# Performance work log

Hardware: AMD Instinct MI355X
Metric: run time of the kernel (lower is better)

The kernel has to match this reference:

```python
import jax, jax.numpy as jnp
import numpy as np

B, L, DIM, H, HD = 2, 2048, 1024, 16, 64


def _rope_tables(L, hd):
    inv_freq = 1.0 / (10000.0 ** (np.arange(0, hd, 2, dtype=np.float32) / hd))
    t = np.arange(L, dtype=np.float32)
    freqs = np.outer(t, inv_freq)                 # [L, hd/2]
    emb = np.concatenate([freqs, freqs], axis=-1)  # [L, hd]
    return jnp.asarray(np.cos(emb)), jnp.asarray(np.sin(emb))


def setup_inputs() -> dict:
    key = jax.random.key(0)
    k1, k2, k3 = jax.random.split(key, 3)
    x = jax.random.normal(k1, (B, L, DIM), dtype=jnp.float32)
    cos, sin = _rope_tables(L, HD)
    w_qkv = jax.random.normal(k2, (DIM, 3 * H * HD), dtype=jnp.float32) * (DIM ** -0.5)
    w_out = jax.random.normal(k3, (H * HD, DIM), dtype=jnp.float32) * ((H * HD) ** -0.5)
    return {"x": x, "cos": cos, "sin": sin, "w_qkv": w_qkv, "w_out": w_out}


def _rotate_half(u):
    u1, u2 = jnp.split(u, 2, axis=-1)
    return jnp.concatenate([-u2, u1], axis=-1)


def _apply_rope(u, cos, sin):
    # u: [B, L, H, hd]; cos/sin: [L, hd]
    c = cos[None, :, None, :]
    s = sin[None, :, None, :]
    return u * c + _rotate_half(u) * s


def reference(x, cos, sin, w_qkv, w_out):
    b, l, _ = x.shape
    qkv = jnp.einsum('bld,de->ble', x, w_qkv).reshape(b, l, 3 * H, HD)
    q, k, v = jnp.split(qkv, 3, axis=2)          # each [B, L, H, hd]
    q = _apply_rope(q, cos, sin)
    k = _apply_rope(k, cos, sin)
    scale = HD ** -0.5                            # SDPA default scale
    scores = jnp.einsum('bqhd,bkhd->bhqk', q, k) * scale
    attn = jax.nn.softmax(scores, axis=-1)
    o = jnp.einsum('bhqk,bkhd->bqhd', attn, v).reshape(b, l, H * HD)
    return jnp.einsum('ble,ed->bld', o, w_out)
```

## Files before the change

### kernel.cpp

```cpp
#include <hip/hip_runtime.h>
#include <hip/hip_bf16.h>

#define BATCH 2
#define SEQ   2048
#define DIM   1024
#define NH    16
#define HD    64
#define K_DIM 1024

typedef __attribute__((ext_vector_type(8))) short short8;
typedef __attribute__((ext_vector_type(4))) short short4v;
typedef __attribute__((ext_vector_type(4))) float f32x4;
typedef unsigned short ushort_t;

__device__ __forceinline__ unsigned short f2b(float x) {
    unsigned int u = __float_as_uint(x);
    u += 0x7FFFu + ((u >> 16) & 1u);
    return (unsigned short)(u >> 16);
}

#define ASYNC_COPY16(gp, lp) \
    __builtin_amdgcn_global_load_lds((const __attribute__((address_space(1))) void*)(gp), \
                                     (__attribute__((address_space(3))) void*)(lp), 16, 0, 0)

__global__ __launch_bounds__(256)
void prep(const float* __restrict__ x, const float* __restrict__ w_qkv,
          const float* __restrict__ w_out, ushort_t* __restrict__ xb,
          ushort_t* __restrict__ wqb, ushort_t* __restrict__ wob)
{
    const int bid = blockIdx.x;
    if (bid < 1024) {
        constexpr int n4 = (BATCH * SEQ * DIM) / 4;
        int i = bid * 256 + threadIdx.x;
        for (; i < n4; i += 1024 * 256) {
            float4 v = ((const float4*)x)[i];
            short4v o;
            o[0] = (short)f2b(v.x); o[1] = (short)f2b(v.y);
            o[2] = (short)f2b(v.z); o[3] = (short)f2b(v.w);
            ((short4v*)xb)[i] = o;
        }
    } else {
        const int lane = threadIdx.x & 63;
        const float* src; ushort_t* dst; int N, job;
        if (bid < 2560) { src = w_qkv; dst = wqb; N = 3072; job = (bid - 1024) * 4 + (threadIdx.x >> 6); }
        else            { src = w_out; dst = wob; N = 1024; job = (bid - 2560) * 4 + (threadIdx.x >> 6); }
        const int jn = (N == 3072) ? (job % 48) : (job % 16);
        const int jk = (N == 3072) ? (job / 48) : (job / 16);
        const int n  = jn * 64 + lane;
        const int k0 = jk * 8;
        short8 o;
        #pragma unroll
        for (int j = 0; j < 8; ++j) o[j] = (short)f2b(src[(size_t)(k0 + j) * N + n]);
        *(short8*)(dst + (size_t)n * K_DIM + k0) = o;
    }
}

__device__ __forceinline__ void gemm_stage(const ushort_t* __restrict__ Ag,
                                           const ushort_t* __restrict__ Bg,
                                           ushort_t* As, ushort_t* Bs,
                                           int k0, int w, int r0, int c0)
{
    ASYNC_COPY16(Ag + (size_t)r0 * K_DIM + k0 + c0 * 8,        As + w * 512);
    ASYNC_COPY16(Ag + (size_t)(64 + r0) * K_DIM + k0 + c0 * 8, As + w * 512 + 2048);
    ASYNC_COPY16(Bg + (size_t)r0 * K_DIM + k0 + c0 * 8,        Bs + w * 512);
    ASYNC_COPY16(Bg + (size_t)(64 + r0) * K_DIM + k0 + c0 * 8, Bs + w * 512 + 2048);
}

__device__ __forceinline__ void mfma_gemm_tile(
    const ushort_t* __restrict__ Ag, const ushort_t* __restrict__ Bg,
    ushort_t (&As)[2][128 * 32], ushort_t (&Bs)[2][128 * 32], f32x4 acc[4][4])
{
    const int t = threadIdx.x;
    const int w = t >> 6, lane = t & 63;
    const int qd = lane >> 4, cl = lane & 15;
    const int p0 = w * 64 + lane;
    const int r0 = p0 >> 2;
    const int c0 = (p0 & 3) ^ (r0 & 3);

    gemm_stage(Ag, Bg, As[0], Bs[0], 0, w, r0, c0);

    for (int kt = 0; kt < K_DIM / 32; ++kt) {
        const int cur = kt & 1;
        __syncthreads();
        if (kt + 1 < K_DIM / 32)
            gemm_stage(Ag, Bg, As[cur ^ 1], Bs[cur ^ 1], (kt + 1) * 32, w, r0, c0);

        short8 af[4], bfr[4];
        #pragma unroll
        for (int rt = 0; rt < 4; ++rt) {
            const int row = (w >> 1) * 64 + rt * 16 + cl;
            af[rt] = *(const short8*)(As[cur] + row * 32 + ((qd ^ (row & 3)) * 8));
        }
        #pragma unroll
        for (int ct = 0; ct < 4; ++ct) {
            const int col = (w & 1) * 64 + ct * 16 + cl;
            bfr[ct] = *(const short8*)(Bs[cur] + col * 32 + ((qd ^ (col & 3)) * 8));
        }
        #pragma unroll
        for (int rt = 0; rt < 4; ++rt)
            #pragma unroll
            for (int ct = 0; ct < 4; ++ct)
                acc[rt][ct] = __builtin_amdgcn_mfma_f32_16x16x32_bf16(
                    af[rt], bfr[ct], acc[rt][ct], 0, 0, 0);
    }
}

__global__ __launch_bounds__(256, 3)
void gemm_qkv_mfma(const ushort_t* __restrict__ xb, const ushort_t* __restrict__ wqb,
                   ushort_t* __restrict__ qb, ushort_t* __restrict__ kb,
                   ushort_t* __restrict__ vt,
                   const float* __restrict__ cosb, const float* __restrict__ sinb)
{
    __shared__ __align__(16) ushort_t As[2][128 * 32];
    __shared__ __align__(16) ushort_t Bs[2][128 * 32];
    const int m0 = blockIdx.y * 128, n0 = blockIdx.x * 128;

    f32x4 acc[4][4];
    #pragma unroll
    for (int i = 0; i < 4; ++i)
        #pragma unroll
        for (int j = 0; j < 4; ++j)
            #pragma unroll
            for (int r = 0; r < 4; ++r) acc[i][j][r] = 0.f;

    mfma_gemm_tile(xb + (size_t)m0 * K_DIM, wqb + (size_t)n0 * K_DIM, As, Bs, acc);

    const int t = threadIdx.x, w = t >> 6, lane = t & 63;
    const int qd = lane >> 4, cl = lane & 15;
    const int b = m0 >> 11;
    const int lbase = (m0 & 2047) + (w >> 1) * 64;
    const int region = blockIdx.x >> 3;
    const int h = (blockIdx.x & 7) * 2 + (w & 1);

    if (region < 2) {
        ushort_t* dst = region ? kb : qb;
        const float sc = region ? 1.0f : 0.18033688011111234f;
        #pragma unroll
        for (int rt = 0; rt < 4; ++rt) {
            #pragma unroll
            for (int r = 0; r < 4; ++r) {
                const int l = lbase + rt * 16 + qd * 4 + r;
                const float c0 = cosb[l * HD + cl],      s0 = sinb[l * HD + cl];
                const float c1 = cosb[l * HD + 16 + cl], s1 = sinb[l * HD + 16 + cl];
                const float v0 = acc[rt][0][r] * c0 - acc[rt][2][r] * s0;
                const float v1 = acc[rt][1][r] * c1 - acc[rt][3][r] * s1;
                const float v2 = acc[rt][2][r] * c0 + acc[rt][0][r] * s0;
                const float v3 = acc[rt][3][r] * c1 + acc[rt][1][r] * s1;
                short4v o4;
                o4[0] = (short)f2b(v0 * sc);
                o4[1] = (short)f2b(v1 * sc);
                o4[2] = (short)f2b(v2 * sc);
                o4[3] = (short)f2b(v3 * sc);
                *(short4v*)(dst + (((size_t)b * NH + h) * SEQ + l) * HD + cl * 4) = o4;
            }
        }
    } else {
        #pragma unroll
        for (int rt = 0; rt < 4; ++rt)
            #pragma unroll
            for (int ct = 0; ct < 4; ++ct) {
                const int d = ct * 16 + cl;
                const int l = lbase + rt * 16 + qd * 4;
                short4v o4;
                #pragma unroll
                for (int r = 0; r < 4; ++r) o4[r] = (short)f2b(acc[rt][ct][r]);
                *(short4v*)(vt + (((size_t)b * NH + h) * HD + d) * SEQ + l) = o4;
            }
    }
}

__device__ __forceinline__ void go_stage(const ushort_t* __restrict__ Ag,
                                         const ushort_t* __restrict__ Bg,
                                         ushort_t* As, ushort_t* Bs,
                                         int k0, int w, int lane)
{
    #pragma unroll
    for (int j = 0; j < 2; ++j) {
        const int r = w * 32 + j * 16 + (lane >> 2);
        const int c = (lane & 3) ^ (r & 3);
        ASYNC_COPY16(Ag + (size_t)r * K_DIM + k0 + c * 8, As + (w * 128 + j * 64) * 8);
    }
    const int rb = w * 16 + (lane >> 2);
    const int cb = (lane & 3) ^ (rb & 3);
    ASYNC_COPY16(Bg + (size_t)rb * K_DIM + k0 + cb * 8, Bs + (w * 64) * 8);
}

__global__ __launch_bounds__(256, 3)
void gemm_out_mfma(const ushort_t* __restrict__ ob, const ushort_t* __restrict__ wob,
                   float* __restrict__ out)
{
    __shared__ __align__(16) ushort_t As[2][128 * 32];
    __shared__ __align__(16) ushort_t Bs[2][64 * 32];
    const int m0 = blockIdx.y * 128, n0 = blockIdx.x * 64;
    const int t = threadIdx.x;
    const int w = t >> 6, lane = t & 63;
    const int qd = lane >> 4, cl = lane & 15;
    const int wr = w >> 1, wc = w & 1;

    f32x4 acc[4][2];
    #pragma unroll
    for (int i = 0; i < 4; ++i)
        #pragma unroll
        for (int j = 0; j < 2; ++j)
            #pragma unroll
            for (int r = 0; r < 4; ++r) acc[i][j][r] = 0.f;

    const ushort_t* Ag = ob  + (size_t)m0 * K_DIM;
    const ushort_t* Bg = wob + (size_t)n0 * K_DIM;
    go_stage(Ag, Bg, As[0], Bs[0], 0, w, lane);

    for (int kt = 0; kt < K_DIM / 32; ++kt) {
        const int cur = kt & 1;
        __syncthreads();
        if (kt + 1 < K_DIM / 32)
            go_stage(Ag, Bg, As[cur ^ 1], Bs[cur ^ 1], (kt + 1) * 32, w, lane);

        short8 af[4], bfr[2];
        #pragma unroll
        for (int rt = 0; rt < 4; ++rt) {
            const int row = wr * 64 + rt * 16 + cl;
            af[rt] = *(const short8*)(As[cur] + row * 32 + ((qd ^ (row & 3)) * 8));
        }
        #pragma unroll
        for (int ct = 0; ct < 2; ++ct) {
            const int col = wc * 32 + ct * 16 + cl;
            bfr[ct] = *(const short8*)(Bs[cur] + col * 32 + ((qd ^ (col & 3)) * 8));
        }
        #pragma unroll
        for (int rt = 0; rt < 4; ++rt)
            #pragma unroll
            for (int ct = 0; ct < 2; ++ct)
                acc[rt][ct] = __builtin_amdgcn_mfma_f32_16x16x32_bf16(
                    af[rt], bfr[ct], acc[rt][ct], 0, 0, 0);
    }

    const int mbase = m0 + wr * 64, nbase = n0 + wc * 32;
    #pragma unroll
    for (int rt = 0; rt < 4; ++rt)
        #pragma unroll
        for (int ct = 0; ct < 2; ++ct)
            #pragma unroll
            for (int r = 0; r < 4; ++r)
                out[(size_t)(mbase + rt * 16 + qd * 4 + r) * DIM + nbase + ct * 16 + cl] =
                    acc[rt][ct][r];
}

__global__ __launch_bounds__(256, 2)
void attn_mfma(const ushort_t* __restrict__ qb, const ushort_t* __restrict__ kb,
               const ushort_t* __restrict__ vt, ushort_t* __restrict__ ob)
{
    const int h = blockIdx.x;
    const int b = blockIdx.y;
    const int qt = blockIdx.z;
    const int t = threadIdx.x;
    const int w = t >> 6, lane = t & 63;
    const int qd = lane >> 4, cl = lane & 15;
    constexpr int NT = SEQ / 64;

    __shared__ __align__(16) ushort_t Ks[2][64 * 64];
    __shared__ __align__(16) ushort_t Vs[2][64 * 64];

    const size_t bh = (size_t)b * NH + h;
    const ushort_t* qbase = qb + (bh * SEQ + qt * 128 + w * 32) * HD;
    const ushort_t* kbase = kb + bh * SEQ * HD;
    const ushort_t* vbase = vt + bh * (size_t)HD * SEQ;

    const int p0 = w * 128 + lane;
    const int r0a = p0 >> 3,  c0a = (p0 & 7) ^ (r0a & 7);
    const int p1 = p0 + 64;
    const int r1a = p1 >> 3,  c1a = (p1 & 7) ^ (r1a & 7);
    const int ldsoff0 = (w * 128) * 8;
    const int ldsoff1 = (w * 128 + 64) * 8;

    const ushort_t* kg0 = kbase + (size_t)r0a * HD + c0a * 8;
    const ushort_t* kg1 = kbase + (size_t)r1a * HD + c1a * 8;
    const ushort_t* vg0 = vbase + (size_t)r0a * SEQ + c0a * 8;
    const ushort_t* vg1 = vbase + (size_t)r1a * SEQ + c1a * 8;

    const int lo0 = (cl * 8 + (qd ^ (cl & 7))) * 8;
    const int lo1 = (cl * 8 + ((4 + qd) ^ (cl & 7))) * 8;
    const ushort_t* kE0 = Ks[0] + lo0; const ushort_t* kE1 = Ks[0] + lo1;
    const ushort_t* vE0 = Vs[0] + lo0; const ushort_t* vE1 = Vs[0] + lo1;
    const ushort_t* kO0 = Ks[1] + lo0; const ushort_t* kO1 = Ks[1] + lo1;
    const ushort_t* vO0 = Vs[1] + lo0; const ushort_t* vO1 = Vs[1] + lo1;

    short8 qf[2][2];
    #pragma unroll
    for (int nt = 0; nt < 2; ++nt)
        #pragma unroll
        for (int kh = 0; kh < 2; ++kh)
            qf[nt][kh] = *(const short8*)(qbase + (nt * 16 + cl) * HD + kh * 32 + qd * 8);

    const f32x4 fz = {0.f, 0.f, 0.f, 0.f};
    short8 onesA;
    #pragma unroll
    for (int e = 0; e < 8; ++e) onesA[e] = (short)0x3F80;

    f32x4 oaccT[4][2];
    f32x4 lacc[2];
    #pragma unroll
    for (int dt = 0; dt < 4; ++dt)
        #pragma unroll
        for (int nt = 0; nt < 2; ++nt)
            #pragma unroll
            for (int r = 0; r < 4; ++r) oaccT[dt][nt][r] = 0.f;
    #pragma unroll
    for (int nt = 0; nt < 2; ++nt)
        #pragma unroll
        for (int r = 0; r < 4; ++r) lacc[nt][r] = 0.f;

    short8 pfE[2][2], vfE[4][2], pfO[2][2], vfO[4][2];
    #pragma unroll
    for (int nt = 0; nt < 2; ++nt)
        #pragma unroll
        for (int kh = 0; kh < 2; ++kh)
            #pragma unroll
            for (int e = 0; e < 8; ++e) pfO[nt][kh][e] = 0;
    #pragma unroll
    for (int dt = 0; dt < 4; ++dt)
        #pragma unroll
        for (int kh = 0; kh < 2; ++kh)
            #pragma unroll
            for (int e = 0; e < 8; ++e) vfO[dt][kh][e] = 0;

    {
        ASYNC_COPY16(kg0, (ushort_t*)Ks[0] + ldsoff0);
        ASYNC_COPY16(kg1, (ushort_t*)Ks[0] + ldsoff1);
        ASYNC_COPY16(vg0, (ushort_t*)Vs[0] + ldsoff0);
        ASYNC_COPY16(vg1, (ushort_t*)Vs[0] + ldsoff1);
        kg0 += 64 * HD; kg1 += 64 * HD; vg0 += 64; vg1 += 64;
    }

    for (int pr = 0; pr < NT / 2; ++pr) {
        __syncthreads();
        {
            ASYNC_COPY16(kg0, (ushort_t*)Ks[1] + ldsoff0);
            ASYNC_COPY16(kg1, (ushort_t*)Ks[1] + ldsoff1);
            ASYNC_COPY16(vg0, (ushort_t*)Vs[1] + ldsoff0);
            ASYNC_COPY16(vg1, (ushort_t*)Vs[1] + ldsoff1);
            kg0 += 64 * HD; kg1 += 64 * HD; vg0 += 64; vg1 += 64;
        }
        {
            short8 kf[4][2];
            #pragma unroll
            for (int mt = 0; mt < 4; ++mt) {
                kf[mt][0] = *(const short8*)(kE0 + mt * 1024);
                kf[mt][1] = *(const short8*)(kE1 + mt * 1024);
            }
            #pragma unroll
            for (int dt = 0; dt < 4; ++dt) {
                vfE[dt][0] = *(const short8*)(vE0 + dt * 1024);
                vfE[dt][1] = *(const short8*)(vE1 + dt * 1024);
            }
            f32x4 s[4][2];
            __builtin_amdgcn_s_setprio(1);
            #pragma unroll
            for (int mt = 0; mt < 4; ++mt)
                #pragma unroll
                for (int nt = 0; nt < 2; ++nt)
                    s[mt][nt] = __builtin_amdgcn_mfma_f32_16x16x32_bf16(
                        kf[mt][0], qf[nt][0], fz, 0, 0, 0);
            #pragma unroll
            for (int mt = 0; mt < 4; ++mt)
                #pragma unroll
                for (int nt = 0; nt < 2; ++nt)
                    s[mt][nt] = __builtin_amdgcn_mfma_f32_16x16x32_bf16(
                        kf[mt][1], qf[nt][1], s[mt][nt], 0, 0, 0);
            #pragma unroll
            for (int kh = 0; kh < 2; ++kh)
                #pragma unroll
                for (int dt = 0; dt < 4; ++dt)
                    #pragma unroll
                    for (int nt = 0; nt < 2; ++nt)
                        oaccT[dt][nt] = __builtin_amdgcn_mfma_f32_16x16x32_bf16(
                            vfO[dt][kh], pfO[nt][kh], oaccT[dt][nt], 0, 0, 0);
            __builtin_amdgcn_s_setprio(0);
            #pragma unroll
            for (int nt = 0; nt < 2; ++nt) {
                unsigned int wr2[4][2];
                #pragma unroll
                for (int mt = 0; mt < 4; ++mt) {
                    const float e0 = __builtin_amdgcn_exp2f(s[mt][nt][0]);
                    const float e1 = __builtin_amdgcn_exp2f(s[mt][nt][1]);
                    const float e2 = __builtin_amdgcn_exp2f(s[mt][nt][2]);
                    const float e3 = __builtin_amdgcn_exp2f(s[mt][nt][3]);
                    union { __hip_bfloat162 h2; unsigned int u; } pk0, pk1;
                    pk0.h2 = __float22bfloat162_rn(make_float2(e0, e1));
                    pk1.h2 = __float22bfloat162_rn(make_float2(e2, e3));
                    wr2[mt][0] = pk0.u;
                    wr2[mt][1] = pk1.u;
                }
                #pragma unroll
                for (int kh = 0; kh < 2; ++kh) {
                    union { unsigned int u[4]; short8 s8; } pu;
                    #pragma unroll
                    for (int i = 0; i < 2; ++i) {
                        unsigned int a  = wr2[2 * kh][i];
                        unsigned int bb = wr2[2 * kh + 1][i];
                        asm("v_permlane32_swap_b32 %0, %1" : "+v"(a), "+v"(bb));
                        asm("v_permlane16_swap_b32 %0, %1" : "+v"(a), "+v"(bb));
                        pu.u[i]     = a;
                        pu.u[2 + i] = bb;
                    }
                    pfE[nt][kh] = pu.s8;
                }
            }
            #pragma unroll
            for (int kh = 0; kh < 2; ++kh)
                #pragma unroll
                for (int nt = 0; nt < 2; ++nt)
                    lacc[nt] = __builtin_amdgcn_mfma_f32_16x16x32_bf16(
                        onesA, pfE[nt][kh], lacc[nt], 0, 0, 0);
        }

        __syncthreads();
        if (pr + 1 < NT / 2) {
            ASYNC_COPY16(kg0, (ushort_t*)Ks[0] + ldsoff0);
            ASYNC_COPY16(kg1, (ushort_t*)Ks[0] + ldsoff1);
            ASYNC_COPY16(vg0, (ushort_t*)Vs[0] + ldsoff0);
            ASYNC_COPY16(vg1, (ushort_t*)Vs[0] + ldsoff1);
            kg0 += 64 * HD; kg1 += 64 * HD; vg0 += 64; vg1 += 64;
        }
        {
            short8 kf[4][2];
            #pragma unroll
            for (int mt = 0; mt < 4; ++mt) {
                kf[mt][0] = *(const short8*)(kO0 + mt * 1024);
                kf[mt][1] = *(const short8*)(kO1 + mt * 1024);
            }
            #pragma unroll
            for (int dt = 0; dt < 4; ++dt) {
                vfO[dt][0] = *(const short8*)(vO0 + dt * 1024);
                vfO[dt][1] = *(const short8*)(vO1 + dt * 1024);
            }
            f32x4 s[4][2];
            __builtin_amdgcn_s_setprio(1);
            #pragma unroll
            for (int mt = 0; mt < 4; ++mt)
                #pragma unroll
                for (int nt = 0; nt < 2; ++nt)
                    s[mt][nt] = __builtin_amdgcn_mfma_f32_16x16x32_bf16(
                        kf[mt][0], qf[nt][0], fz, 0, 0, 0);
            #pragma unroll
            for (int mt = 0; mt < 4; ++mt)
                #pragma unroll
                for (int nt = 0; nt < 2; ++nt)
                    s[mt][nt] = __builtin_amdgcn_mfma_f32_16x16x32_bf16(
                        kf[mt][1], qf[nt][1], s[mt][nt], 0, 0, 0);
            #pragma unroll
            for (int kh = 0; kh < 2; ++kh)
                #pragma unroll
                for (int dt = 0; dt < 4; ++dt)
                    #pragma unroll
                    for (int nt = 0; nt < 2; ++nt)
                        oaccT[dt][nt] = __builtin_amdgcn_mfma_f32_16x16x32_bf16(
                            vfE[dt][kh], pfE[nt][kh], oaccT[dt][nt], 0, 0, 0);
            __builtin_amdgcn_s_setprio(0);
            #pragma unroll
            for (int nt = 0; nt < 2; ++nt) {
                unsigned int wr2[4][2];
                #pragma unroll
                for (int mt = 0; mt < 4; ++mt) {
                    const float e0 = __builtin_amdgcn_exp2f(s[mt][nt][0]);
                    const float e1 = __builtin_amdgcn_exp2f(s[mt][nt][1]);
                    const float e2 = __builtin_amdgcn_exp2f(s[mt][nt][2]);
                    const float e3 = __builtin_amdgcn_exp2f(s[mt][nt][3]);
                    union { __hip_bfloat162 h2; unsigned int u; } pk0, pk1;
                    pk0.h2 = __float22bfloat162_rn(make_float2(e0, e1));
                    pk1.h2 = __float22bfloat162_rn(make_float2(e2, e3));
                    wr2[mt][0] = pk0.u;
                    wr2[mt][1] = pk1.u;
                }
                #pragma unroll
                for (int kh = 0; kh < 2; ++kh) {
                    union { unsigned int u[4]; short8 s8; } pu;
                    #pragma unroll
                    for (int i = 0; i < 2; ++i) {
                        unsigned int a  = wr2[2 * kh][i];
                        unsigned int bb = wr2[2 * kh + 1][i];
                        asm("v_permlane32_swap_b32 %0, %1" : "+v"(a), "+v"(bb));
                        asm("v_permlane16_swap_b32 %0, %1" : "+v"(a), "+v"(bb));
                        pu.u[i]     = a;
                        pu.u[2 + i] = bb;
                    }
                    pfO[nt][kh] = pu.s8;
                }
            }
            #pragma unroll
            for (int kh = 0; kh < 2; ++kh)
                #pragma unroll
                for (int nt = 0; nt < 2; ++nt)
                    lacc[nt] = __builtin_amdgcn_mfma_f32_16x16x32_bf16(
                        onesA, pfO[nt][kh], lacc[nt], 0, 0, 0);
        }
    }

    #pragma unroll
    for (int kh = 0; kh < 2; ++kh)
        #pragma unroll
        for (int dt = 0; dt < 4; ++dt)
            #pragma unroll
            for (int nt = 0; nt < 2; ++nt)
                oaccT[dt][nt] = __builtin_amdgcn_mfma_f32_16x16x32_bf16(
                    vfO[dt][kh], pfO[nt][kh], oaccT[dt][nt], 0, 0, 0);

    #pragma unroll
    for (int nt = 0; nt < 2; ++nt) {
        const float inv = 1.0f / lacc[nt][0];
        const int query = qt * 128 + w * 32 + nt * 16 + cl;
        ushort_t* op = ob + ((size_t)b * SEQ + query) * DIM + h * HD;
        #pragma unroll
        for (int dt = 0; dt < 4; ++dt) {
            short4v o4;
            #pragma unroll
            for (int r = 0; r < 4; ++r) o4[r] = (short)f2b(oaccT[dt][nt][r] * inv);
            *(short4v*)(op + dt * 16 + qd * 4) = o4;
        }
    }
}

extern "C" void kernel_launch(void* const* d_in, const int* in_sizes, int n_in,
                              void* d_out, int out_size, void* d_ws, size_t ws_size,
                              hipStream_t stream)
{
    const float* x     = (const float*)d_in[0];
    const float* cosb  = (const float*)d_in[1];
    const float* sinb  = (const float*)d_in[2];
    const float* w_qkv = (const float*)d_in[3];
    const float* w_out = (const float*)d_in[4];
    float* out = (float*)d_out;

    constexpr size_t MB = 1u << 20;
    char* ws = (char*)d_ws;
    ushort_t* qb  = (ushort_t*)(ws);
    ushort_t* kb  = (ushort_t*)(ws + 8 * MB);
    ushort_t* vt  = (ushort_t*)(ws + 16 * MB);
    ushort_t* wob = (ushort_t*)(ws + 24 * MB);
    ushort_t* ob  = (ushort_t*)(ws + 26 * MB);
    ushort_t* xb  = (ushort_t*)(ws + 34 * MB);
    ushort_t* wqb = (ushort_t*)(ws + 42 * MB);

    prep<<<3072, 256, 0, stream>>>(x, w_qkv, w_out, xb, wqb, wob);
    gemm_qkv_mfma<<<dim3(24, 32), 256, 0, stream>>>(xb, wqb, qb, kb, vt, cosb, sinb);
    attn_mfma<<<dim3(16, 2, 16), 256, 0, stream>>>(qb, kb, vt, ob);
    gemm_out_mfma<<<dim3(16, 32), 256, 0, stream>>>(ob, wob, out);
}
```

Baseline: 191.0 us.

## Split attention over key halves with a combine kernel; restructure GEMM k-loops

The attention kernel now splits the key/value sequence into two halves, one per block, which doubles the grid to 1024 blocks and raises the occupancy hint to 4. Each half writes its normalized partial output and row-sum to workspace, and a new reduce_o kernel merges them weighted by the row-sums. This relies on the softmax there not subtracting a running max, so the sums can be combined directly. Separately, both GEMM k-loops are unrolled by two, with LDS addresses precomputed and fragment loads issued before the next async stage. The costs are an extra kernel launch, extra workspace traffic reusing the xb/wqb buffers, and a second bf16 rounding of the output.

```diff
diff --git a/kernel.cpp b/kernel.cpp
--- a/kernel.cpp
+++ b/kernel.cpp
@@ -17,6 +17,10 @@
     unsigned int u = __float_as_uint(x);
     u += 0x7FFFu + ((u >> 16) & 1u);
     return (unsigned short)(u >> 16);
+}
+
+__device__ __forceinline__ float b2f(unsigned short u) {
+    return __uint_as_float(((unsigned int)u) << 16);
 }
 
 #define ASYNC_COPY16(gp, lp) \
@@ -77,31 +81,53 @@
     const int r0 = p0 >> 2;
     const int c0 = (p0 & 3) ^ (r0 & 3);
 
+    const ushort_t* aB[4];
+    const ushort_t* bB[4];
+    #pragma unroll
+    for (int rt = 0; rt < 4; ++rt) {
+        const int row = (w >> 1) * 64 + rt * 16 + cl;
+        aB[rt] = As[0] + row * 32 + ((qd ^ (row & 3)) * 8);
+    }
+    #pragma unroll
+    for (int ct = 0; ct < 4; ++ct) {
+        const int col = (w & 1) * 64 + ct * 16 + cl;
+        bB[ct] = Bs[0] + col * 32 + ((qd ^ (col & 3)) * 8);
+    }
+
     gemm_stage(Ag, Bg, As[0], Bs[0], 0, w, r0, c0);
 
-    for (int kt = 0; kt < K_DIM / 32; ++kt) {
-        const int cur = kt & 1;
+    for (int kp = 0; kp < K_DIM / 64; ++kp) {
         __syncthreads();
-        if (kt + 1 < K_DIM / 32)
-            gemm_stage(Ag, Bg, As[cur ^ 1], Bs[cur ^ 1], (kt + 1) * 32, w, r0, c0);
-
-        short8 af[4], bfr[4];
-        #pragma unroll
-        for (int rt = 0; rt < 4; ++rt) {
-            const int row = (w >> 1) * 64 + rt * 16 + cl;
-            af[rt] = *(const short8*)(As[cur] + row * 32 + ((qd ^ (row & 3)) * 8));
-        }
-        #pragma unroll
-        for (int ct = 0; ct < 4; ++ct) {
-            const int col = (w & 1) * 64 + ct * 16 + cl;
-            bfr[ct] = *(const short8*)(Bs[cur] + col * 32 + ((qd ^ (col & 3)) * 8));
-        }
-        #pragma unroll
-        for (int rt = 0; rt < 4; ++rt)
-            #pragma unroll
-            for (int ct = 0; ct < 4; ++ct)
-                acc[rt][ct] = __builtin_amdgcn_mfma_f32_16x16x32_bf16(
-                    af[rt], bfr[ct], acc[rt][ct], 0, 0, 0);
+        {
+            short8 af[4], bfr[4];
+            #pragma unroll
+            for (int rt = 0; rt < 4; ++rt) af[rt] = *(const short8*)(aB[rt]);
+            #pragma unroll
+            for (int ct = 0; ct < 4; ++ct) bfr[ct] = *(const short8*)(bB[ct]);
+            gemm_stage(Ag, Bg, As[1], Bs[1], kp * 64 + 32, w, r0, c0);
+            #pragma unroll
+            for (int rt = 0; rt < 4; ++rt)
+                #pragma unroll
+                for (int ct = 0; ct < 4; ++ct)
+                    acc[rt][ct] = __builtin_amdgcn_mfma_f32_16x16x32_bf16(
+                        af[rt], bfr[ct], acc[rt][ct], 0, 0, 0);
+        }
+        __syncthreads();
+        {
+            short8 af[4], bfr[4];
+            #pragma unroll
+            for (int rt = 0; rt < 4; ++rt) af[rt] = *(const short8*)(aB[rt] + 4096);
+            #pragma unroll
+            for (int ct = 0; ct < 4; ++ct) bfr[ct] = *(const short8*)(bB[ct] + 4096);
+            if (kp + 1 < K_DIM / 64)
+                gemm_stage(Ag, Bg, As[0], Bs[0], kp * 64 + 64, w, r0, c0);
+            #pragma unroll
+            for (int rt = 0; rt < 4; ++rt)
+                #pragma unroll
+                for (int ct = 0; ct < 4; ++ct)
+                    acc[rt][ct] = __builtin_amdgcn_mfma_f32_16x16x32_bf16(
+                        af[rt], bfr[ct], acc[rt][ct], 0, 0, 0);
+        }
     }
 }
 
@@ -207,31 +233,54 @@
 
     const ushort_t* Ag = ob  + (size_t)m0 * K_DIM;
     const ushort_t* Bg = wob + (size_t)n0 * K_DIM;
+
+    const ushort_t* aB[4];
+    const ushort_t* bB[2];
+    #pragma unroll
+    for (int rt = 0; rt < 4; ++rt) {
+        const int row = wr * 64 + rt * 16 + cl;
+        aB[rt] = As[0] + row * 32 + ((qd ^ (row & 3)) * 8);
+    }
+    #pragma unroll
+    for (int ct = 0; ct < 2; ++ct) {
+        const int col = wc * 32 + ct * 16 + cl;
+        bB[ct] = Bs[0] + col * 32 + ((qd ^ (col & 3)) * 8);
+    }
+
     go_stage(Ag, Bg, As[0], Bs[0], 0, w, lane);
 
-    for (int kt = 0; kt < K_DIM / 32; ++kt) {
-        const int cur = kt & 1;
+    for (int kp = 0; kp < K_DIM / 64; ++kp) {
         __syncthreads();
-        if (kt + 1 < K_DIM / 32)
-            go_stage(Ag, Bg, As[cur ^ 1], Bs[cur ^ 1], (kt + 1) * 32, w, lane);
-
-        short8 af[4], bfr[2];
-        #pragma unroll
-        for (int rt = 0; rt < 4; ++rt) {
-            const int row = wr * 64 + rt * 16 + cl;
-            af[rt] = *(const short8*)(As[cur] + row * 32 + ((qd ^ (row & 3)) * 8));
-        }
-        #pragma unroll
-        for (int ct = 0; ct < 2; ++ct) {
-            const int col = wc * 32 + ct * 16 + cl;
-            bfr[ct] = *(const short8*)(Bs[cur] + col * 32 + ((qd ^ (col & 3)) * 8));
-        }
-        #pragma unroll
-        for (int rt = 0; rt < 4; ++rt)
-            #pragma unroll
-            for (int ct = 0; ct < 2; ++ct)
-                acc[rt][ct] = __builtin_amdgcn_mfma_f32_16x16x32_bf16(
-                    af[rt], bfr[ct], acc[rt][ct], 0, 0, 0);
+        {
+            short8 af[4], bfr[2];
+            #pragma unroll
+            for (int rt = 0; rt < 4; ++rt) af[rt] = *(const short8*)(aB[rt]);
+            #pragma unroll
+            for (int ct = 0; ct < 2; ++ct) bfr[ct] = *(const short8*)(bB[ct]);
+            go_stage(Ag, Bg, As[1], Bs[1], kp * 64 + 32, w, lane);
+            #pragma unroll
+            for (int rt = 0; rt < 4; ++rt)
+                #pragma unroll
+                for (int ct = 0; ct < 2; ++ct)
+                    acc[rt][ct] = __builtin_amdgcn_mfma_f32_16x16x32_bf16(
+                        af[rt], bfr[ct], acc[rt][ct], 0, 0, 0);
+        }
+        __syncthreads();
+        {
+            short8 af[4], bfr[2];
+            #pragma unroll
+            for (int rt = 0; rt < 4; ++rt) af[rt] = *(const short8*)(aB[rt] + 4096);
+            #pragma unroll
+            for (int ct = 0; ct < 2; ++ct) bfr[ct] = *(const short8*)(bB[ct] + 2048);
+            if (kp + 1 < K_DIM / 64)
+                go_stage(Ag, Bg, As[0], Bs[0], kp * 64 + 64, w, lane);
+            #pragma unroll
+            for (int rt = 0; rt < 4; ++rt)
+                #pragma unroll
+                for (int ct = 0; ct < 2; ++ct)
+                    acc[rt][ct] = __builtin_amdgcn_mfma_f32_16x16x32_bf16(
+                        af[rt], bfr[ct], acc[rt][ct], 0, 0, 0);
+        }
     }
 
     const int mbase = m0 + wr * 64, nbase = n0 + wc * 32;
@@ -245,17 +294,19 @@
                     acc[rt][ct][r];
 }
 
-__global__ __launch_bounds__(256, 2)
+__global__ __launch_bounds__(256, 4)
 void attn_mfma(const ushort_t* __restrict__ qb, const ushort_t* __restrict__ kb,
-               const ushort_t* __restrict__ vt, ushort_t* __restrict__ ob)
+               const ushort_t* __restrict__ vt, ushort_t* __restrict__ o1b,
+               ushort_t* __restrict__ o2b, float* __restrict__ lbuf)
 {
     const int h = blockIdx.x;
     const int b = blockIdx.y;
-    const int qt = blockIdx.z;
+    const int qt = blockIdx.z >> 1;
+    const int half = blockIdx.z & 1;
     const int t = threadIdx.x;
     const int w = t >> 6, lane = t & 63;
     const int qd = lane >> 4, cl = lane & 15;
-    constexpr int NT = SEQ / 64;
+    constexpr int NTL = 16;
 
     __shared__ __align__(16) ushort_t Ks[2][64 * 64];
     __shared__ __align__(16) ushort_t Vs[2][64 * 64];
@@ -272,10 +323,10 @@
     const int ldsoff0 = (w * 128) * 8;
     const int ldsoff1 = (w * 128 + 64) * 8;
 
-    const ushort_t* kg0 = kbase + (size_t)r0a * HD + c0a * 8;
-    const ushort_t* kg1 = kbase + (size_t)r1a * HD + c1a * 8;
-    const ushort_t* vg0 = vbase + (size_t)r0a * SEQ + c0a * 8;
-    const ushort_t* vg1 = vbase + (size_t)r1a * SEQ + c1a * 8;
+    const ushort_t* kg0 = kbase + (size_t)(half * NTL * 64 + r0a) * HD + c0a * 8;
+    const ushort_t* kg1 = kbase + (size_t)(half * NTL * 64 + r1a) * HD + c1a * 8;
+    const ushort_t* vg0 = vbase + (size_t)r0a * SEQ + half * NTL * 64 + c0a * 8;
+    const ushort_t* vg1 = vbase + (size_t)r1a * SEQ + half * NTL * 64 + c1a * 8;
 
     const int lo0 = (cl * 8 + (qd ^ (cl & 7))) * 8;
     const int lo1 = (cl * 8 + ((4 + qd) ^ (cl & 7))) * 8;
@@ -331,7 +382,7 @@
         kg0 += 64 * HD; kg1 += 64 * HD; vg0 += 64; vg1 += 64;
     }
 
-    for (int pr = 0; pr < NT / 2; ++pr) {
+    for (int pr = 0; pr < NTL / 2; ++pr) {
         __syncthreads();
         {
             ASYNC_COPY16(kg0, (ushort_t*)Ks[1] + ldsoff0);
@@ -414,7 +465,7 @@
         }
 
         __syncthreads();
-        if (pr + 1 < NT / 2) {
+        if (pr + 1 < NTL / 2) {
             ASYNC_COPY16(kg0, (ushort_t*)Ks[0] + ldsoff0);
             ASYNC_COPY16(kg1, (ushort_t*)Ks[0] + ldsoff1);
             ASYNC_COPY16(vg0, (ushort_t*)Vs[0] + ldsoff0);
@@ -504,11 +555,13 @@
                 oaccT[dt][nt] = __builtin_amdgcn_mfma_f32_16x16x32_bf16(
                     vfO[dt][kh], pfO[nt][kh], oaccT[dt][nt], 0, 0, 0);
 
+    ushort_t* dst = half ? o2b : o1b;
     #pragma unroll
     for (int nt = 0; nt < 2; ++nt) {
-        const float inv = 1.0f / lacc[nt][0];
+        const float l = lacc[nt][0];
+        const float inv = 1.0f / l;
         const int query = qt * 128 + w * 32 + nt * 16 + cl;
-        ushort_t* op = ob + ((size_t)b * SEQ + query) * DIM + h * HD;
+        ushort_t* op = dst + ((size_t)b * SEQ + query) * DIM + h * HD;
         #pragma unroll
         for (int dt = 0; dt < 4; ++dt) {
             short4v o4;
@@ -516,7 +569,30 @@
             for (int r = 0; r < 4; ++r) o4[r] = (short)f2b(oaccT[dt][nt][r] * inv);
             *(short4v*)(op + dt * 16 + qd * 4) = o4;
         }
-    }
+        if (qd == 0)
+            lbuf[(((size_t)half * BATCH + b) * NH + h) * SEQ + query] = l;
+    }
+}
+
+__global__ __launch_bounds__(256)
+void reduce_o(const ushort_t* o1, const ushort_t* o2,
+              const float* __restrict__ lbuf, ushort_t* ob)
+{
+    const int idx = blockIdx.x * 256 + threadIdx.x;
+    const int h = (idx >> 3) & 15;
+    const int q = (idx >> 7) & 2047;
+    const int b = idx >> 18;
+    const float l1 = lbuf[((size_t)(b * NH + h)) * SEQ + q];
+    const float l2 = lbuf[(size_t)BATCH * NH * SEQ + ((size_t)(b * NH + h)) * SEQ + q];
+    const float inv = 1.0f / (l1 + l2);
+    const float a1 = l1 * inv, a2 = l2 * inv;
+    const short8 v1 = *(const short8*)(o1 + (size_t)idx * 8);
+    const short8 v2 = *(const short8*)(o2 + (size_t)idx * 8);
+    short8 o;
+    #pragma unroll
+    for (int e = 0; e < 8; ++e)
+        o[e] = (short)f2b(a1 * b2f((ushort_t)v1[e]) + a2 * b2f((ushort_t)v2[e]));
+    *(short8*)(ob + (size_t)idx * 8) = o;
 }
 
 extern "C" void kernel_launch(void* const* d_in, const int* in_sizes, int n_in,
@@ -539,9 +615,12 @@
     ushort_t* ob  = (ushort_t*)(ws + 26 * MB);
     ushort_t* xb  = (ushort_t*)(ws + 34 * MB);
     ushort_t* wqb = (ushort_t*)(ws + 42 * MB);
+    ushort_t* o2b  = xb;
+    float*    lbuf = (float*)wqb;
 
     prep<<<3072, 256, 0, stream>>>(x, w_qkv, w_out, xb, wqb, wob);
     gemm_qkv_mfma<<<dim3(24, 32), 256, 0, stream>>>(xb, wqb, qb, kb, vt, cosb, sinb);
-    attn_mfma<<<dim3(16, 2, 16), 256, 0, stream>>>(qb, kb, vt, ob);
+    attn_mfma<<<dim3(16, 2, 32), 256, 0, stream>>>(qb, kb, vt, ob, o2b, lbuf);
+    reduce_o<<<2048, 256, 0, stream>>>(ob, o2b, lbuf, ob);
     gemm_out_mfma<<<dim3(16, 32), 256, 0, stream>>>(ob, wob, out);
 }
```

After: 387.1 us. 103% more time.
